# Kernel tuning notes

Measured on AMD Instinct MI355X. Metric: run time of the kernel, lower is better.

Reference implementation:

```python
import jax, jax.numpy as jnp
import numpy as np

D_MODEL = 256
N_HEADS = 8


def setup_inputs() -> dict:
    key = jax.random.key(0)
    ks = jax.random.split(key, 12)
    B, S, d, H = 4, 1024, D_MODEL, N_HEADS
    s = 0.02
    return {
        "Q": jax.random.normal(ks[0], (B, S, d), jnp.float32),
        "K": jax.random.normal(ks[1], (B, S, d), jnp.float32),
        "V": jax.random.normal(ks[2], (B, S, d), jnp.float32),
        "Wq": jax.random.normal(ks[3], (d, d * H), jnp.float32) * s,
        "bq": jnp.zeros((d * H,), jnp.float32),
        "Wk": jax.random.normal(ks[4], (d, d * H), jnp.float32) * s,
        "bk": jnp.zeros((d * H,), jnp.float32),
        "Wv": jax.random.normal(ks[5], (d, d * H), jnp.float32) * s,
        "bv": jnp.zeros((d * H,), jnp.float32),
        "Wo": jax.random.normal(ks[6], (H * d, d), jnp.float32) * s,
        "bo": jnp.zeros((d,), jnp.float32),
    }


def reference(Q, K, V, Wq, bq, Wk, bk, Wv, bv, Wo, bo):
    B, S, d = Q.shape
    H = N_HEADS
    # projections: [B,S,d] -> [B,S,H*d] -> [B,H,S,d] (head_dim == d_model here)
    q = (Q @ Wq + bq).reshape(B, S, H, d).transpose(0, 2, 1, 3)
    k = (K @ Wk + bk).reshape(B, S, H, d).transpose(0, 2, 1, 3)
    v = (V @ Wv + bv).reshape(B, S, H, d).transpose(0, 2, 1, 3)
    scores = jnp.einsum("bhqd,bhkd->bhqk", q, k) / jnp.sqrt(jnp.float32(d))
    attn = jax.nn.softmax(scores, axis=-1)
    out = jnp.einsum("bhqk,bhkd->bhqd", attn, v)  # [B,H,S,d]
    out = out.transpose(0, 2, 1, 3).reshape(B, S, H * d)
    return out @ Wo + bo
```

## Files before the change

### kernel.cpp

```cpp
#include <hip/hip_runtime.h>
#include <stdint.h>

#define NB 4
#define SEQ 1024
#define DM 256
#define NH 8

typedef __attribute__((ext_vector_type(8))) short bf8;
typedef __attribute__((ext_vector_type(4))) float f4;

__device__ __forceinline__ unsigned short f2bf(float f) {
  union { float f; uint32_t u; } c; c.f = f;
  uint32_t u = c.u;
  return (unsigned short)((u + 0x7FFFu + ((u >> 16) & 1u)) >> 16);
}

__device__ __forceinline__ void gl_lds16(const unsigned short* g, short* l) {
  __builtin_amdgcn_global_load_lds(
      (const __attribute__((address_space(1))) unsigned int*)g,
      (__attribute__((address_space(3))) unsigned int*)l, 16, 0, 0);
}


__global__ __launch_bounds__(256) void prep_kernel(
    const float* __restrict__ Wq, const float* __restrict__ Wk,
    const float* __restrict__ Wv, const float* __restrict__ Wo,
    const float* __restrict__ Q, const float* __restrict__ K,
    const float* __restrict__ V,
    unsigned short* __restrict__ Wt3, unsigned short* __restrict__ WoT,
    unsigned short* __restrict__ Xbf) {
  const int tid = threadIdx.x;
  const int bid = blockIdx.x;

#pragma unroll
  for (int it = 0; it < 6; ++it) {
    const int idx = (it * 512 + bid) * 256 + tid;
    const int z = idx >> 18;
    const int r = idx & 262143;
    const float* src = (z == 0) ? Q : (z == 1) ? K : V;
    const float4 v = *(const float4*)(src + (size_t)r * 4);
    short4 s;
    s.x = (short)f2bf(v.x); s.y = (short)f2bf(v.y);
    s.z = (short)f2bf(v.z); s.w = (short)f2bf(v.w);
    *(short4*)(Xbf + (size_t)z * 1048576 + (size_t)r * 4) = s;
  }

  __shared__ float t[32][33];
  const int tx = tid & 31, ty = tid >> 5;
  for (int tt = 0; tt < 4; ++tt) {
    const int id = bid * 4 + tt;
    const float* in;
    unsigned short* out;
    int R, C, bx, by;
    if (id < 1536) {
      const int z = id >> 9, rem = id & 511;
      in = (z == 0) ? Wq : (z == 1) ? Wk : Wv;
      out = Wt3 + (size_t)z * 2048 * 256;
      R = 256; C = 2048; bx = rem & 63; by = rem >> 6;
    } else {
      const int rem = id - 1536;
      in = Wo; out = WoT;
      R = 2048; C = 256; bx = rem & 7; by = rem >> 3;
    }
    const int c0 = bx * 32, r0 = by * 32;
    __syncthreads();
#pragma unroll
    for (int i = 0; i < 4; i++) {
      int r = r0 + ty + i * 8;
      t[ty + i * 8][tx] = in[(size_t)r * C + c0 + tx];
    }
    __syncthreads();
#pragma unroll
    for (int i = 0; i < 4; i++) {
      int c = c0 + ty + i * 8;
      out[(size_t)c * R + r0 + tx] = f2bf(t[tx][ty + i * 8]);
    }
  }
}

__global__ __launch_bounds__(256) void proj_kernel(
    const unsigned short* __restrict__ Xbf, const unsigned short* __restrict__ Wt3,
    const float* __restrict__ bq, const float* __restrict__ bk, const float* __restrict__ bv,
    unsigned short* __restrict__ q_frag, unsigned short* __restrict__ k_frag,
    unsigned short* __restrict__ v_frag) {
  const int z = blockIdx.z;
  const unsigned short* X = Xbf + (size_t)z * 4096 * 256;
  const unsigned short* Wt = Wt3 + (size_t)z * 2048 * 256;
  const float* bias = (z == 0) ? bq : (z == 1) ? bk : bv;

  __shared__ short a_lds[128 * 64];
  __shared__ short b_lds[128 * 64];

  const int tid = threadIdx.x;
  const int wid = tid >> 6, lane = tid & 63;
  const int quad = lane >> 4, l16 = lane & 15;
  const int wm = wid >> 1, wn = wid & 1;
  const int m0 = blockIdx.x * 128, n0 = blockIdx.y * 128;

  f4 acc[4][4];
  const f4 z4 = {0.f, 0.f, 0.f, 0.f};
#pragma unroll
  for (int i = 0; i < 4; i++)
#pragma unroll
    for (int j = 0; j < 4; j++) acc[i][j] = z4;

  const int srow = lane >> 2;
  const int schunk = lane & 3;
  const int cxor = quad ^ (l16 & 3);

  for (int ko = 0; ko < 4; ko++) {
    const int k0 = ko * 64;
#pragma unroll
    for (int jj = 0; jj < 4; jj++) {
      const int c = wid * 4 + jj;
      const int kh = c >> 3, i = c & 7;
      const int row = i * 16 + srow;
      const int sc = (schunk ^ (row & 3)) * 8;
      gl_lds16(X + (size_t)(m0 + row) * DM + k0 + kh * 32 + sc, a_lds + c * 512);
      gl_lds16(Wt + (size_t)(n0 + row) * DM + k0 + kh * 32 + sc, b_lds + c * 512);
    }
    __syncthreads();
#pragma unroll
    for (int kh = 0; kh < 2; kh++) {
      bf8 af[4], bfv[4];
#pragma unroll
      for (int mi = 0; mi < 4; mi++)
        af[mi] = *(const bf8*)(a_lds + kh * 4096 + (wm * 64 + mi * 16 + l16) * 32 + cxor * 8);
#pragma unroll
      for (int ni = 0; ni < 4; ni++)
        bfv[ni] = *(const bf8*)(b_lds + kh * 4096 + (wn * 64 + ni * 16 + l16) * 32 + cxor * 8);
      if (z < 2) {
#pragma unroll
        for (int ni = 0; ni < 4; ni++)
#pragma unroll
          for (int mi = 0; mi < 4; mi++)
            acc[ni][mi] = __builtin_amdgcn_mfma_f32_16x16x32_bf16(bfv[ni], af[mi], acc[ni][mi], 0, 0, 0);
      } else {
#pragma unroll
        for (int mi = 0; mi < 4; mi++)
#pragma unroll
          for (int ni = 0; ni < 4; ni++)
            acc[mi][ni] = __builtin_amdgcn_mfma_f32_16x16x32_bf16(af[mi], bfv[ni], acc[mi][ni], 0, 0, 0);
      }
    }
    __syncthreads();
  }

  if (z < 2) {
    const float scale = (z == 0) ? 0.0901684400f : 1.0f;
    unsigned short* dst = (z == 0) ? q_frag : k_frag;
#pragma unroll
    for (int ni = 0; ni < 4; ni++) {
      const int nb = n0 + wn * 64 + ni * 16 + quad * 4;
      const float4 b4 = *(const float4*)(bias + nb);
      const int h = nb >> 8, dd = nb & 255;
      const int dq = (dd >> 3) & 3, jh = dd & 7;
#pragma unroll
      for (int mi = 0; mi < 4; mi++) {
        const int tok = m0 + wm * 64 + mi * 16 + l16;
        const int b = tok >> 10, sr = tok & 1023;
        const size_t idx = ((size_t)(b * NH + h) * 64 + (sr >> 4)) * 4096 +
                           (size_t)(dd >> 5) * 512 + ((sr & 15) + 16 * dq) * 8 + jh;
        short4 s4;
        s4.x = (short)f2bf((acc[ni][mi][0] + b4.x) * scale);
        s4.y = (short)f2bf((acc[ni][mi][1] + b4.y) * scale);
        s4.z = (short)f2bf((acc[ni][mi][2] + b4.z) * scale);
        s4.w = (short)f2bf((acc[ni][mi][3] + b4.w) * scale);
        *(short4*)(dst + idx) = s4;
      }
    }
  } else {
#pragma unroll
    for (int ni = 0; ni < 4; ni++) {
      const int n = n0 + wn * 64 + ni * 16 + l16;
      const float bsv = bias[n];
      const int h = n >> 8, d = n & 255;
#pragma unroll
      for (int mi = 0; mi < 4; mi++) {
        const int m = m0 + wm * 64 + mi * 16 + quad * 4;
        const int b = m >> 10, sr = m & 1023;
        const size_t idx = ((size_t)(b * NH + h) * 16 + (d >> 4)) * 16384 +
                           (size_t)(sr >> 5) * 512 +
                           ((d & 15) + 16 * ((sr >> 3) & 3)) * 8 + (sr & 7);
        short4 s4;
        s4.x = (short)f2bf(acc[mi][ni][0] + bsv);
        s4.y = (short)f2bf(acc[mi][ni][1] + bsv);
        s4.z = (short)f2bf(acc[mi][ni][2] + bsv);
        s4.w = (short)f2bf(acc[mi][ni][3] + bsv);
        *(short4*)(v_frag + idx) = s4;
      }
    }
  }
}

__global__ __launch_bounds__(256) void attn_kernel(
    const unsigned short* __restrict__ q_frag, const unsigned short* __restrict__ k_frag,
    const unsigned short* __restrict__ v_frag, unsigned short* __restrict__ o_ws) {
  __shared__ short k_lds[2][8192];
  __shared__ short p_lds[2][64][40];
  __shared__ float l_sh[64];

  const int tid = threadIdx.x;
  const int wid = tid >> 6, lane = tid & 63;
  const int quad = lane >> 4, l16 = lane & 15;
  const int blk = blockIdx.x;
  const int g = blk & 7;
  const int qt = (blk >> 3) & 15;
  const int bh = g + 8 * (blk >> 7);
  const size_t fbase = (size_t)bh * 262144;

  bf8 qf[8];
  {
    const unsigned short* qp = q_frag + fbase + (size_t)(qt * 4 + wid) * 4096 + lane * 8;
#pragma unroll
    for (int kc = 0; kc < 8; kc++) qf[kc] = *(const bf8*)(qp + kc * 512);
  }

  const f4 z4 = {0.f, 0.f, 0.f, 0.f};
  f4 Oacc[4][4];
#pragma unroll
  for (int i = 0; i < 4; i++)
#pragma unroll
    for (int j = 0; j < 4; j++) Oacc[i][j] = z4;
  float lpart[4] = {0.f, 0.f, 0.f, 0.f};

  const unsigned short* kdma_src = k_frag + fbase + (size_t)wid * 2048 + lane * 8;
#pragma unroll
  for (int jj = 0; jj < 4; jj++)
    gl_lds16(kdma_src + jj * 512, &k_lds[0][wid * 2048 + jj * 512]);
  __syncthreads();

  bf8 vpre0[4], vpre1[4];
  const unsigned short* vbase_p = v_frag + fbase + (size_t)(wid * 4) * 16384 + lane * 8;

#define ATTN_STEP(T, CUR, PRV, VCUR, VPRV)                                     \
  {                                                                            \
    const int t_ = (T);                                                        \
    _Pragma("unroll")                                                          \
    for (int mi = 0; mi < 4; mi++)                                             \
      VCUR[mi] = *(const bf8*)(vbase_p + (size_t)mi * 16384 + (size_t)t_ * 512); \
    f4 Sacc[2];                                                                \
    Sacc[0] = z4; Sacc[1] = z4;                                                \
    _Pragma("unroll")                                                          \
    for (int kc = 0; kc < 8; kc++) {                                           \
      const bf8 aq = qf[kc];                                                   \
      _Pragma("unroll")                                                        \
      for (int ni = 0; ni < 2; ni++) {                                         \
        const bf8 kb = *(const bf8*)(&k_lds[CUR][(ni * 8 + kc) * 512 + lane * 8]); \
        Sacc[ni] = __builtin_amdgcn_mfma_f32_16x16x32_bf16(aq, kb, Sacc[ni], 0, 0, 0); \
      }                                                                        \
    }                                                                          \
    if (t_ < 31) {                                                             \
      _Pragma("unroll")                                                        \
      for (int jj = 0; jj < 4; jj++)                                           \
        gl_lds16(kdma_src + (size_t)(t_ + 1) * 8192 + jj * 512,                \
                 &k_lds[PRV][wid * 2048 + jj * 512]);                          \
    }                                                                          \
    if (t_ > 0) {                                                              \
      bf8 pb[4];                                                               \
      _Pragma("unroll")                                                        \
      for (int nq = 0; nq < 4; nq++)                                           \
        pb[nq] = *(const bf8*)(&p_lds[PRV][nq * 16 + l16][quad * 8]);          \
      _Pragma("unroll")                                                        \
      for (int mi = 0; mi < 4; mi++)                                           \
        _Pragma("unroll")                                                      \
        for (int nq = 0; nq < 4; nq++)                                         \
          Oacc[mi][nq] = __builtin_amdgcn_mfma_f32_16x16x32_bf16(VPRV[mi], pb[nq], Oacc[mi][nq], 0, 0, 0); \
    }                                                                          \
    _Pragma("unroll")                                                          \
    for (int reg = 0; reg < 4; reg++) {                                        \
      const int qrow = wid * 16 + quad * 4 + reg;                              \
      float s = 0.f;                                                           \
      _Pragma("unroll")                                                        \
      for (int ni = 0; ni < 2; ni++) {                                         \
        const float p = exp2f(Sacc[ni][reg]);                                  \
        s += p;                                                                \
        union { float f; uint32_t u; } c;                                      \
        c.f = p;                                                               \
        p_lds[CUR][qrow][ni * 16 + l16] = (short)((c.u + 0x8000u) >> 16);      \
      }                                                                        \
      lpart[reg] += s;                                                         \
    }                                                                          \
    __syncthreads();                                                           \
  }

  for (int tt = 0; tt < 16; tt++) {
    ATTN_STEP(tt * 2, 0, 1, vpre0, vpre1)
    ATTN_STEP(tt * 2 + 1, 1, 0, vpre1, vpre0)
  }
#undef ATTN_STEP

  {
    bf8 pb[4];
#pragma unroll
    for (int nq = 0; nq < 4; nq++)
      pb[nq] = *(const bf8*)(&p_lds[1][nq * 16 + l16][quad * 8]);
#pragma unroll
    for (int mi = 0; mi < 4; mi++)
#pragma unroll
      for (int nq = 0; nq < 4; nq++)
        Oacc[mi][nq] = __builtin_amdgcn_mfma_f32_16x16x32_bf16(vpre1[mi], pb[nq], Oacc[mi][nq], 0, 0, 0);
  }

#pragma unroll
  for (int reg = 0; reg < 4; reg++) {
    float v = lpart[reg];
    v += __shfl_xor(v, 1, 64);
    v += __shfl_xor(v, 2, 64);
    v += __shfl_xor(v, 4, 64);
    v += __shfl_xor(v, 8, 64);
    if (l16 == 0) l_sh[wid * 16 + quad * 4 + reg] = v;
  }
  __syncthreads();

  const int b = bh >> 3, h = bh & 7;
#pragma unroll
  for (int nq = 0; nq < 4; nq++) {
    const int q = nq * 16 + l16;
    const float inv = 1.f / l_sh[q];
    const size_t base = ((size_t)b * SEQ + qt * 64 + q) * (NH * DM) + h * DM + wid * 64;
#pragma unroll
    for (int mi = 0; mi < 4; mi++) {
      short4 s4;
      s4.x = (short)f2bf(Oacc[mi][nq][0] * inv);
      s4.y = (short)f2bf(Oacc[mi][nq][1] * inv);
      s4.z = (short)f2bf(Oacc[mi][nq][2] * inv);
      s4.w = (short)f2bf(Oacc[mi][nq][3] * inv);
      *(short4*)(o_ws + base + mi * 16 + quad * 4) = s4;
    }
  }
}

__global__ __launch_bounds__(256) void outproj_kernel(
    const unsigned short* __restrict__ o_ws, const unsigned short* __restrict__ WoT,
    const float* __restrict__ bo, float* __restrict__ out) {
  __shared__ short a_lds[32][264];
  __shared__ short b_lds[64][264];

  const int tid = threadIdx.x;
  const int wid = tid >> 6, lane = tid & 63;
  const int quad = lane >> 4, l16 = lane & 15;
  const int wm = wid & 1, wn = wid >> 1;
  const int m0 = blockIdx.x * 32, n0 = blockIdx.y * 64;

  const f4 z4 = {0.f, 0.f, 0.f, 0.f};
  f4 acc[2];
#pragma unroll
  for (int i = 0; i < 2; i++) acc[i] = z4;

  const int ch = tid & 31, row = tid >> 5;
  for (int ko = 0; ko < 8; ko++) {
    const int k0 = ko * 256;
#pragma unroll
    for (int rb = 0; rb < 4; rb++) {
      int r = row + rb * 8;
      *(bf8*)(&a_lds[r][ch * 8]) = *(const bf8*)(o_ws + (size_t)(m0 + r) * 2048 + k0 + ch * 8);
    }
#pragma unroll
    for (int rb = 0; rb < 8; rb++) {
      int r = row + rb * 8;
      *(bf8*)(&b_lds[r][ch * 8]) = *(const bf8*)(WoT + (size_t)(n0 + r) * 2048 + k0 + ch * 8);
    }
    __syncthreads();
#pragma unroll
    for (int kc = 0; kc < 8; kc++) {
      const bf8 af = *(const bf8*)(&a_lds[wm * 16 + l16][kc * 32 + quad * 8]);
      bf8 bfv[2];
#pragma unroll
      for (int ni = 0; ni < 2; ni++)
        bfv[ni] = *(const bf8*)(&b_lds[wn * 32 + ni * 16 + l16][kc * 32 + quad * 8]);
#pragma unroll
      for (int ni = 0; ni < 2; ni++)
        acc[ni] = __builtin_amdgcn_mfma_f32_16x16x32_bf16(af, bfv[ni], acc[ni], 0, 0, 0);
    }
    __syncthreads();
  }
#pragma unroll
  for (int ni = 0; ni < 2; ni++) {
    const int n = n0 + wn * 32 + ni * 16 + l16;
    const float bv = bo[n];
#pragma unroll
    for (int reg = 0; reg < 4; reg++) {
      const int m = m0 + wm * 16 + quad * 4 + reg;
      out[(size_t)m * DM + n] = acc[ni][reg] + bv;
    }
  }
}

extern "C" void kernel_launch(void* const* d_in, const int* in_sizes, int n_in,
                              void* d_out, int out_size, void* d_ws, size_t ws_size,
                              hipStream_t stream) {
  const float* Q  = (const float*)d_in[0];
  const float* K  = (const float*)d_in[1];
  const float* V  = (const float*)d_in[2];
  const float* Wq = (const float*)d_in[3];
  const float* bq = (const float*)d_in[4];
  const float* Wk = (const float*)d_in[5];
  const float* bk = (const float*)d_in[6];
  const float* Wv = (const float*)d_in[7];
  const float* bv = (const float*)d_in[8];
  const float* Wo = (const float*)d_in[9];
  const float* bo = (const float*)d_in[10];
  float* out = (float*)d_out;

  char* ws = (char*)d_ws;
  const size_t QS = (size_t)NB * NH * SEQ * DM * 2;
  unsigned short* q_frag = (unsigned short*)(ws);
  unsigned short* k_frag = (unsigned short*)(ws + QS);
  unsigned short* v_frag = (unsigned short*)(ws + 2 * QS);
  unsigned short* o_ws   = (unsigned short*)(ws + 3 * QS);
  const size_t WT = (size_t)2048 * 256 * 2;
  unsigned short* Wt3 = (unsigned short*)(ws + 4 * QS);
  unsigned short* WoT = (unsigned short*)(ws + 4 * QS + 3 * WT);
  unsigned short* Xbf = o_ws;

  prep_kernel<<<512, 256, 0, stream>>>(Wq, Wk, Wv, Wo, Q, K, V,
                                       Wt3, WoT, Xbf);
  proj_kernel<<<dim3(32, 16, 3), 256, 0, stream>>>(Xbf, Wt3, bq, bk, bv,
                                                   q_frag, k_frag, v_frag);
  attn_kernel<<<512, 256, 0, stream>>>(q_frag, k_frag, v_frag, o_ws);
  outproj_kernel<<<dim3(128, 4), 256, 0, stream>>>(o_ws, WoT, bo, out);
}
```

Before: 166.9 us.

## Fuse four kernels into one persistent kernel with grid barriers

```diff
diff --git a/kernel.cpp b/kernel.cpp
--- a/kernel.cpp
+++ b/kernel.cpp
@@ -21,217 +21,230 @@
       (__attribute__((address_space(3))) unsigned int*)l, 16, 0, 0);
 }
 
-
-__global__ __launch_bounds__(256) void prep_kernel(
-    const float* __restrict__ Wq, const float* __restrict__ Wk,
-    const float* __restrict__ Wv, const float* __restrict__ Wo,
-    const float* __restrict__ Q, const float* __restrict__ K,
-    const float* __restrict__ V,
-    unsigned short* __restrict__ Wt3, unsigned short* __restrict__ WoT,
-    unsigned short* __restrict__ Xbf) {
+__device__ __forceinline__ void grid_barrier(unsigned* cnt, unsigned nblk) {
+  __threadfence();
+  __syncthreads();
+  if (threadIdx.x == 0) {
+    atomicAdd(cnt, 1u);
+    unsigned spins = 0;
+    while (atomicAdd(cnt, 0u) < nblk) {
+      __builtin_amdgcn_s_sleep(8);
+      if (++spins > 10000000u) break;
+    }
+  }
+  __syncthreads();
+  __threadfence();
+}
+
+union SMemU {
+  struct { float t[32][33]; } prep;
+  struct { short a[128 * 64]; short b[128 * 64]; } proj;
+  struct { short k[2][8192]; short p[2][64][40]; float l[64]; } attn;
+  struct { short a[32][136]; short b[64][136]; } oproj;
+};
+
+__global__ __launch_bounds__(256, 2) void fused_kernel(
+    const float* Wq, const float* Wk, const float* Wv, const float* Wo,
+    const float* Q, const float* K, const float* V,
+    const float* bq, const float* bk, const float* bv, const float* bo,
+    unsigned short* Wt3, unsigned short* WoT, unsigned short* Xbf,
+    unsigned short* q_frag, unsigned short* k_frag, unsigned short* v_frag,
+    unsigned short* o_ws, float* out, unsigned* bar) {
+  __shared__ alignas(16) SMemU sm;
+
   const int tid = threadIdx.x;
   const int bid = blockIdx.x;
-
-#pragma unroll
-  for (int it = 0; it < 6; ++it) {
-    const int idx = (it * 512 + bid) * 256 + tid;
-    const int z = idx >> 18;
-    const int r = idx & 262143;
-    const float* src = (z == 0) ? Q : (z == 1) ? K : V;
-    const float4 v = *(const float4*)(src + (size_t)r * 4);
-    short4 s;
-    s.x = (short)f2bf(v.x); s.y = (short)f2bf(v.y);
-    s.z = (short)f2bf(v.z); s.w = (short)f2bf(v.w);
-    *(short4*)(Xbf + (size_t)z * 1048576 + (size_t)r * 4) = s;
-  }
-
-  __shared__ float t[32][33];
-  const int tx = tid & 31, ty = tid >> 5;
-  for (int tt = 0; tt < 4; ++tt) {
-    const int id = bid * 4 + tt;
-    const float* in;
-    unsigned short* out;
-    int R, C, bx, by;
-    if (id < 1536) {
-      const int z = id >> 9, rem = id & 511;
-      in = (z == 0) ? Wq : (z == 1) ? Wk : Wv;
-      out = Wt3 + (size_t)z * 2048 * 256;
-      R = 256; C = 2048; bx = rem & 63; by = rem >> 6;
-    } else {
-      const int rem = id - 1536;
-      in = Wo; out = WoT;
-      R = 2048; C = 256; bx = rem & 7; by = rem >> 3;
-    }
-    const int c0 = bx * 32, r0 = by * 32;
-    __syncthreads();
-#pragma unroll
-    for (int i = 0; i < 4; i++) {
-      int r = r0 + ty + i * 8;
-      t[ty + i * 8][tx] = in[(size_t)r * C + c0 + tx];
-    }
-    __syncthreads();
-#pragma unroll
-    for (int i = 0; i < 4; i++) {
-      int c = c0 + ty + i * 8;
-      out[(size_t)c * R + r0 + tx] = f2bf(t[tx][ty + i * 8]);
-    }
-  }
-}
-
-__global__ __launch_bounds__(256) void proj_kernel(
-    const unsigned short* __restrict__ Xbf, const unsigned short* __restrict__ Wt3,
-    const float* __restrict__ bq, const float* __restrict__ bk, const float* __restrict__ bv,
-    unsigned short* __restrict__ q_frag, unsigned short* __restrict__ k_frag,
-    unsigned short* __restrict__ v_frag) {
-  const int z = blockIdx.z;
-  const unsigned short* X = Xbf + (size_t)z * 4096 * 256;
-  const unsigned short* Wt = Wt3 + (size_t)z * 2048 * 256;
-  const float* bias = (z == 0) ? bq : (z == 1) ? bk : bv;
-
-  __shared__ short a_lds[128 * 64];
-  __shared__ short b_lds[128 * 64];
-
-  const int tid = threadIdx.x;
   const int wid = tid >> 6, lane = tid & 63;
   const int quad = lane >> 4, l16 = lane & 15;
-  const int wm = wid >> 1, wn = wid & 1;
-  const int m0 = blockIdx.x * 128, n0 = blockIdx.y * 128;
-
-  f4 acc[4][4];
   const f4 z4 = {0.f, 0.f, 0.f, 0.f};
-#pragma unroll
-  for (int i = 0; i < 4; i++)
-#pragma unroll
-    for (int j = 0; j < 4; j++) acc[i][j] = z4;
-
-  const int srow = lane >> 2;
-  const int schunk = lane & 3;
-  const int cxor = quad ^ (l16 & 3);
-
-  for (int ko = 0; ko < 4; ko++) {
-    const int k0 = ko * 64;
-#pragma unroll
-    for (int jj = 0; jj < 4; jj++) {
-      const int c = wid * 4 + jj;
-      const int kh = c >> 3, i = c & 7;
-      const int row = i * 16 + srow;
-      const int sc = (schunk ^ (row & 3)) * 8;
-      gl_lds16(X + (size_t)(m0 + row) * DM + k0 + kh * 32 + sc, a_lds + c * 512);
-      gl_lds16(Wt + (size_t)(n0 + row) * DM + k0 + kh * 32 + sc, b_lds + c * 512);
-    }
+
+  {
+#pragma unroll
+    for (int it = 0; it < 6; ++it) {
+      const int idx = (it * 512 + bid) * 256 + tid;
+      const int z = idx >> 18;
+      const int r = idx & 262143;
+      const float* src = (z == 0) ? Q : (z == 1) ? K : V;
+      const float4 v = *(const float4*)(src + (size_t)r * 4);
+      short4 s;
+      s.x = (short)f2bf(v.x); s.y = (short)f2bf(v.y);
+      s.z = (short)f2bf(v.z); s.w = (short)f2bf(v.w);
+      *(short4*)(Xbf + (size_t)z * 1048576 + (size_t)r * 4) = s;
+    }
+    float (*t)[33] = sm.prep.t;
+    const int tx = tid & 31, ty = tid >> 5;
+    for (int tt = 0; tt < 4; ++tt) {
+      const int id = bid * 4 + tt;
+      const float* in;
+      unsigned short* outp;
+      int R, C, bx, by;
+      if (id < 1536) {
+        const int z = id >> 9, rem = id & 511;
+        in = (z == 0) ? Wq : (z == 1) ? Wk : Wv;
+        outp = Wt3 + (size_t)z * 2048 * 256;
+        R = 256; C = 2048; bx = rem & 63; by = rem >> 6;
+      } else {
+        const int rem = id - 1536;
+        in = Wo; outp = WoT;
+        R = 2048; C = 256; bx = rem & 7; by = rem >> 3;
+      }
+      const int c0 = bx * 32, r0 = by * 32;
+      __syncthreads();
+#pragma unroll
+      for (int i = 0; i < 4; i++) {
+        int r = r0 + ty + i * 8;
+        t[ty + i * 8][tx] = in[(size_t)r * C + c0 + tx];
+      }
+      __syncthreads();
+#pragma unroll
+      for (int i = 0; i < 4; i++) {
+        int c = c0 + ty + i * 8;
+        outp[(size_t)c * R + r0 + tx] = f2bf(t[tx][ty + i * 8]);
+      }
+    }
+  }
+  grid_barrier(bar + 0, 512);
+
+  {
+    short* a_lds = sm.proj.a;
+    short* b_lds = sm.proj.b;
+    const int bx = bid & 31, by = bid >> 5;
+    const int m0 = bx * 128, n0 = by * 128;
+    const int wm = wid >> 1, wn = wid & 1;
+    const int srow = lane >> 2, schunk = lane & 3;
+    const int cxor = quad ^ (l16 & 3);
+
+    for (int z = 0; z < 3; z++) {
+      const unsigned short* X = Xbf + (size_t)z * 1048576;
+      const unsigned short* Wt = Wt3 + (size_t)z * 524288;
+      const float* bias = (z == 0) ? bq : (z == 1) ? bk : bv;
+
+      f4 acc[4][4];
+#pragma unroll
+      for (int i = 0; i < 4; i++)
+#pragma unroll
+        for (int j = 0; j < 4; j++) acc[i][j] = z4;
+
+      for (int ko = 0; ko < 4; ko++) {
+        const int k0 = ko * 64;
+#pragma unroll
+        for (int jj = 0; jj < 4; jj++) {
+          const int c = wid * 4 + jj;
+          const int kh = c >> 3, i = c & 7;
+          const int row = i * 16 + srow;
+          const int sc = (schunk ^ (row & 3)) * 8;
+          gl_lds16(X + (size_t)(m0 + row) * DM + k0 + kh * 32 + sc, a_lds + c * 512);
+          gl_lds16(Wt + (size_t)(n0 + row) * DM + k0 + kh * 32 + sc, b_lds + c * 512);
+        }
+        __syncthreads();
+#pragma unroll
+        for (int kh = 0; kh < 2; kh++) {
+          bf8 af[4], bfv[4];
+#pragma unroll
+          for (int mi = 0; mi < 4; mi++)
+            af[mi] = *(const bf8*)(a_lds + kh * 4096 + (wm * 64 + mi * 16 + l16) * 32 + cxor * 8);
+#pragma unroll
+          for (int ni = 0; ni < 4; ni++)
+            bfv[ni] = *(const bf8*)(b_lds + kh * 4096 + (wn * 64 + ni * 16 + l16) * 32 + cxor * 8);
+          if (z < 2) {
+#pragma unroll
+            for (int ni = 0; ni < 4; ni++)
+#pragma unroll
+              for (int mi = 0; mi < 4; mi++)
+                acc[ni][mi] = __builtin_amdgcn_mfma_f32_16x16x32_bf16(bfv[ni], af[mi], acc[ni][mi], 0, 0, 0);
+          } else {
+#pragma unroll
+            for (int mi = 0; mi < 4; mi++)
+#pragma unroll
+              for (int ni = 0; ni < 4; ni++)
+                acc[mi][ni] = __builtin_amdgcn_mfma_f32_16x16x32_bf16(af[mi], bfv[ni], acc[mi][ni], 0, 0, 0);
+          }
+        }
+        __syncthreads();
+      }
+
+      if (z < 2) {
+        const float scale = (z == 0) ? 0.0901684400f : 1.0f;
+        unsigned short* dst = (z == 0) ? q_frag : k_frag;
+#pragma unroll
+        for (int ni = 0; ni < 4; ni++) {
+          const int nb = n0 + wn * 64 + ni * 16 + quad * 4;
+          const float4 b4 = *(const float4*)(bias + nb);
+          const int h = nb >> 8, dd = nb & 255;
+          const int dq = (dd >> 3) & 3, jh = dd & 7;
+#pragma unroll
+          for (int mi = 0; mi < 4; mi++) {
+            const int tok = m0 + wm * 64 + mi * 16 + l16;
+            const int b = tok >> 10, sr = tok & 1023;
+            const size_t idx = ((size_t)(b * NH + h) * 64 + (sr >> 4)) * 4096 +
+                               (size_t)(dd >> 5) * 512 + ((sr & 15) + 16 * dq) * 8 + jh;
+            short4 s4;
+            s4.x = (short)f2bf((acc[ni][mi][0] + b4.x) * scale);
+            s4.y = (short)f2bf((acc[ni][mi][1] + b4.y) * scale);
+            s4.z = (short)f2bf((acc[ni][mi][2] + b4.z) * scale);
+            s4.w = (short)f2bf((acc[ni][mi][3] + b4.w) * scale);
+            *(short4*)(dst + idx) = s4;
+          }
+        }
+      } else {
+#pragma unroll
+        for (int ni = 0; ni < 4; ni++) {
+          const int n = n0 + wn * 64 + ni * 16 + l16;
+          const float bsv = bias[n];
+          const int h = n >> 8, d = n & 255;
+#pragma unroll
+          for (int mi = 0; mi < 4; mi++) {
+            const int m = m0 + wm * 64 + mi * 16 + quad * 4;
+            const int b = m >> 10, sr = m & 1023;
+            const size_t idx = ((size_t)(b * NH + h) * 16 + (d >> 4)) * 16384 +
+                               (size_t)(sr >> 5) * 512 +
+                               ((d & 15) + 16 * ((sr >> 3) & 3)) * 8 + (sr & 7);
+            short4 s4;
+            s4.x = (short)f2bf(acc[mi][ni][0] + bsv);
+            s4.y = (short)f2bf(acc[mi][ni][1] + bsv);
+            s4.z = (short)f2bf(acc[mi][ni][2] + bsv);
+            s4.w = (short)f2bf(acc[mi][ni][3] + bsv);
+            *(short4*)(v_frag + idx) = s4;
+          }
+        }
+      }
+    }
+  }
+  grid_barrier(bar + 1, 512);
+
+  {
+    short (*k_lds)[8192] = sm.attn.k;
+    short (*p_lds)[64][40] = sm.attn.p;
+    float* l_sh = sm.attn.l;
+
+    const int blk = bid;
+    const int g = blk & 7;
+    const int qt = (blk >> 3) & 15;
+    const int bh = g + 8 * (blk >> 7);
+    const size_t fbase = (size_t)bh * 262144;
+
+    bf8 qf[8];
+    {
+      const unsigned short* qp = q_frag + fbase + (size_t)(qt * 4 + wid) * 4096 + lane * 8;
+#pragma unroll
+      for (int kc = 0; kc < 8; kc++) qf[kc] = *(const bf8*)(qp + kc * 512);
+    }
+
+    f4 Oacc[4][4];
+#pragma unroll
+    for (int i = 0; i < 4; i++)
+#pragma unroll
+      for (int j = 0; j < 4; j++) Oacc[i][j] = z4;
+    float lpart[4] = {0.f, 0.f, 0.f, 0.f};
+
+    const unsigned short* kdma_src = k_frag + fbase + (size_t)wid * 2048 + lane * 8;
+#pragma unroll
+    for (int jj = 0; jj < 4; jj++)
+      gl_lds16(kdma_src + jj * 512, &k_lds[0][wid * 2048 + jj * 512]);
     __syncthreads();
-#pragma unroll
-    for (int kh = 0; kh < 2; kh++) {
-      bf8 af[4], bfv[4];
-#pragma unroll
-      for (int mi = 0; mi < 4; mi++)
-        af[mi] = *(const bf8*)(a_lds + kh * 4096 + (wm * 64 + mi * 16 + l16) * 32 + cxor * 8);
-#pragma unroll
-      for (int ni = 0; ni < 4; ni++)
-        bfv[ni] = *(const bf8*)(b_lds + kh * 4096 + (wn * 64 + ni * 16 + l16) * 32 + cxor * 8);
-      if (z < 2) {
-#pragma unroll
-        for (int ni = 0; ni < 4; ni++)
-#pragma unroll
-          for (int mi = 0; mi < 4; mi++)
-            acc[ni][mi] = __builtin_amdgcn_mfma_f32_16x16x32_bf16(bfv[ni], af[mi], acc[ni][mi], 0, 0, 0);
-      } else {
-#pragma unroll
-        for (int mi = 0; mi < 4; mi++)
-#pragma unroll
-          for (int ni = 0; ni < 4; ni++)
-            acc[mi][ni] = __builtin_amdgcn_mfma_f32_16x16x32_bf16(af[mi], bfv[ni], acc[mi][ni], 0, 0, 0);
-      }
-    }
-    __syncthreads();
-  }
-
-  if (z < 2) {
-    const float scale = (z == 0) ? 0.0901684400f : 1.0f;
-    unsigned short* dst = (z == 0) ? q_frag : k_frag;
-#pragma unroll
-    for (int ni = 0; ni < 4; ni++) {
-      const int nb = n0 + wn * 64 + ni * 16 + quad * 4;
-      const float4 b4 = *(const float4*)(bias + nb);
-      const int h = nb >> 8, dd = nb & 255;
-      const int dq = (dd >> 3) & 3, jh = dd & 7;
-#pragma unroll
-      for (int mi = 0; mi < 4; mi++) {
-        const int tok = m0 + wm * 64 + mi * 16 + l16;
-        const int b = tok >> 10, sr = tok & 1023;
-        const size_t idx = ((size_t)(b * NH + h) * 64 + (sr >> 4)) * 4096 +
-                           (size_t)(dd >> 5) * 512 + ((sr & 15) + 16 * dq) * 8 + jh;
-        short4 s4;
-        s4.x = (short)f2bf((acc[ni][mi][0] + b4.x) * scale);
-        s4.y = (short)f2bf((acc[ni][mi][1] + b4.y) * scale);
-        s4.z = (short)f2bf((acc[ni][mi][2] + b4.z) * scale);
-        s4.w = (short)f2bf((acc[ni][mi][3] + b4.w) * scale);
-        *(short4*)(dst + idx) = s4;
-      }
-    }
-  } else {
-#pragma unroll
-    for (int ni = 0; ni < 4; ni++) {
-      const int n = n0 + wn * 64 + ni * 16 + l16;
-      const float bsv = bias[n];
-      const int h = n >> 8, d = n & 255;
-#pragma unroll
-      for (int mi = 0; mi < 4; mi++) {
-        const int m = m0 + wm * 64 + mi * 16 + quad * 4;
-        const int b = m >> 10, sr = m & 1023;
-        const size_t idx = ((size_t)(b * NH + h) * 16 + (d >> 4)) * 16384 +
-                           (size_t)(sr >> 5) * 512 +
-                           ((d & 15) + 16 * ((sr >> 3) & 3)) * 8 + (sr & 7);
-        short4 s4;
-        s4.x = (short)f2bf(acc[mi][ni][0] + bsv);
-        s4.y = (short)f2bf(acc[mi][ni][1] + bsv);
-        s4.z = (short)f2bf(acc[mi][ni][2] + bsv);
-        s4.w = (short)f2bf(acc[mi][ni][3] + bsv);
-        *(short4*)(v_frag + idx) = s4;
-      }
-    }
-  }
-}
-
-__global__ __launch_bounds__(256) void attn_kernel(
-    const unsigned short* __restrict__ q_frag, const unsigned short* __restrict__ k_frag,
-    const unsigned short* __restrict__ v_frag, unsigned short* __restrict__ o_ws) {
-  __shared__ short k_lds[2][8192];
-  __shared__ short p_lds[2][64][40];
-  __shared__ float l_sh[64];
-
-  const int tid = threadIdx.x;
-  const int wid = tid >> 6, lane = tid & 63;
-  const int quad = lane >> 4, l16 = lane & 15;
-  const int blk = blockIdx.x;
-  const int g = blk & 7;
-  const int qt = (blk >> 3) & 15;
-  const int bh = g + 8 * (blk >> 7);
-  const size_t fbase = (size_t)bh * 262144;
-
-  bf8 qf[8];
-  {
-    const unsigned short* qp = q_frag + fbase + (size_t)(qt * 4 + wid) * 4096 + lane * 8;
-#pragma unroll
-    for (int kc = 0; kc < 8; kc++) qf[kc] = *(const bf8*)(qp + kc * 512);
-  }
-
-  const f4 z4 = {0.f, 0.f, 0.f, 0.f};
-  f4 Oacc[4][4];
-#pragma unroll
-  for (int i = 0; i < 4; i++)
-#pragma unroll
-    for (int j = 0; j < 4; j++) Oacc[i][j] = z4;
-  float lpart[4] = {0.f, 0.f, 0.f, 0.f};
-
-  const unsigned short* kdma_src = k_frag + fbase + (size_t)wid * 2048 + lane * 8;
-#pragma unroll
-  for (int jj = 0; jj < 4; jj++)
-    gl_lds16(kdma_src + jj * 512, &k_lds[0][wid * 2048 + jj * 512]);
-  __syncthreads();
-
-  bf8 vpre0[4], vpre1[4];
-  const unsigned short* vbase_p = v_frag + fbase + (size_t)(wid * 4) * 16384 + lane * 8;
+
+    bf8 vpre0[4], vpre1[4];
+    const unsigned short* vbase_p = v_frag + fbase + (size_t)(wid * 4) * 16384 + lane * 8;
 
 #define ATTN_STEP(T, CUR, PRV, VCUR, VPRV)                                     \
   {                                                                            \
@@ -284,105 +297,101 @@
     __syncthreads();                                                           \
   }
 
-  for (int tt = 0; tt < 16; tt++) {
-    ATTN_STEP(tt * 2, 0, 1, vpre0, vpre1)
-    ATTN_STEP(tt * 2 + 1, 1, 0, vpre1, vpre0)
-  }
+    for (int tt = 0; tt < 16; tt++) {
+      ATTN_STEP(tt * 2, 0, 1, vpre0, vpre1)
+      ATTN_STEP(tt * 2 + 1, 1, 0, vpre1, vpre0)
+    }
 #undef ATTN_STEP
 
+    {
+      bf8 pb[4];
+#pragma unroll
+      for (int nq = 0; nq < 4; nq++)
+        pb[nq] = *(const bf8*)(&p_lds[1][nq * 16 + l16][quad * 8]);
+#pragma unroll
+      for (int mi = 0; mi < 4; mi++)
+#pragma unroll
+        for (int nq = 0; nq < 4; nq++)
+          Oacc[mi][nq] = __builtin_amdgcn_mfma_f32_16x16x32_bf16(vpre1[mi], pb[nq], Oacc[mi][nq], 0, 0, 0);
+    }
+
+#pragma unroll
+    for (int reg = 0; reg < 4; reg++) {
+      float v = lpart[reg];
+      v += __shfl_xor(v, 1, 64);
+      v += __shfl_xor(v, 2, 64);
+      v += __shfl_xor(v, 4, 64);
+      v += __shfl_xor(v, 8, 64);
+      if (l16 == 0) l_sh[wid * 16 + quad * 4 + reg] = v;
+    }
+    __syncthreads();
+
+    const int b = bh >> 3, h = bh & 7;
+#pragma unroll
+    for (int nq = 0; nq < 4; nq++) {
+      const int q = nq * 16 + l16;
+      const float inv = 1.f / l_sh[q];
+      const size_t base = ((size_t)b * SEQ + qt * 64 + q) * (NH * DM) + h * DM + wid * 64;
+#pragma unroll
+      for (int mi = 0; mi < 4; mi++) {
+        short4 s4;
+        s4.x = (short)f2bf(Oacc[mi][nq][0] * inv);
+        s4.y = (short)f2bf(Oacc[mi][nq][1] * inv);
+        s4.z = (short)f2bf(Oacc[mi][nq][2] * inv);
+        s4.w = (short)f2bf(Oacc[mi][nq][3] * inv);
+        *(short4*)(o_ws + base + mi * 16 + quad * 4) = s4;
+      }
+    }
+  }
+  grid_barrier(bar + 2, 512);
+
   {
-    bf8 pb[4];
-#pragma unroll
-    for (int nq = 0; nq < 4; nq++)
-      pb[nq] = *(const bf8*)(&p_lds[1][nq * 16 + l16][quad * 8]);
-#pragma unroll
-    for (int mi = 0; mi < 4; mi++)
-#pragma unroll
-      for (int nq = 0; nq < 4; nq++)
-        Oacc[mi][nq] = __builtin_amdgcn_mfma_f32_16x16x32_bf16(vpre1[mi], pb[nq], Oacc[mi][nq], 0, 0, 0);
-  }
-
-#pragma unroll
-  for (int reg = 0; reg < 4; reg++) {
-    float v = lpart[reg];
-    v += __shfl_xor(v, 1, 64);
-    v += __shfl_xor(v, 2, 64);
-    v += __shfl_xor(v, 4, 64);
-    v += __shfl_xor(v, 8, 64);
-    if (l16 == 0) l_sh[wid * 16 + quad * 4 + reg] = v;
-  }
-  __syncthreads();
-
-  const int b = bh >> 3, h = bh & 7;
-#pragma unroll
-  for (int nq = 0; nq < 4; nq++) {
-    const int q = nq * 16 + l16;
-    const float inv = 1.f / l_sh[q];
-    const size_t base = ((size_t)b * SEQ + qt * 64 + q) * (NH * DM) + h * DM + wid * 64;
-#pragma unroll
-    for (int mi = 0; mi < 4; mi++) {
-      short4 s4;
-      s4.x = (short)f2bf(Oacc[mi][nq][0] * inv);
-      s4.y = (short)f2bf(Oacc[mi][nq][1] * inv);
-      s4.z = (short)f2bf(Oacc[mi][nq][2] * inv);
-      s4.w = (short)f2bf(Oacc[mi][nq][3] * inv);
-      *(short4*)(o_ws + base + mi * 16 + quad * 4) = s4;
-    }
-  }
-}
-
-__global__ __launch_bounds__(256) void outproj_kernel(
-    const unsigned short* __restrict__ o_ws, const unsigned short* __restrict__ WoT,
-    const float* __restrict__ bo, float* __restrict__ out) {
-  __shared__ short a_lds[32][264];
-  __shared__ short b_lds[64][264];
-
-  const int tid = threadIdx.x;
-  const int wid = tid >> 6, lane = tid & 63;
-  const int quad = lane >> 4, l16 = lane & 15;
-  const int wm = wid & 1, wn = wid >> 1;
-  const int m0 = blockIdx.x * 32, n0 = blockIdx.y * 64;
-
-  const f4 z4 = {0.f, 0.f, 0.f, 0.f};
-  f4 acc[2];
-#pragma unroll
-  for (int i = 0; i < 2; i++) acc[i] = z4;
-
-  const int ch = tid & 31, row = tid >> 5;
-  for (int ko = 0; ko < 8; ko++) {
-    const int k0 = ko * 256;
-#pragma unroll
-    for (int rb = 0; rb < 4; rb++) {
-      int r = row + rb * 8;
-      *(bf8*)(&a_lds[r][ch * 8]) = *(const bf8*)(o_ws + (size_t)(m0 + r) * 2048 + k0 + ch * 8);
-    }
-#pragma unroll
-    for (int rb = 0; rb < 8; rb++) {
-      int r = row + rb * 8;
-      *(bf8*)(&b_lds[r][ch * 8]) = *(const bf8*)(WoT + (size_t)(n0 + r) * 2048 + k0 + ch * 8);
-    }
-    __syncthreads();
-#pragma unroll
-    for (int kc = 0; kc < 8; kc++) {
-      const bf8 af = *(const bf8*)(&a_lds[wm * 16 + l16][kc * 32 + quad * 8]);
-      bf8 bfv[2];
-#pragma unroll
-      for (int ni = 0; ni < 2; ni++)
-        bfv[ni] = *(const bf8*)(&b_lds[wn * 32 + ni * 16 + l16][kc * 32 + quad * 8]);
-#pragma unroll
-      for (int ni = 0; ni < 2; ni++)
-        acc[ni] = __builtin_amdgcn_mfma_f32_16x16x32_bf16(af, bfv[ni], acc[ni], 0, 0, 0);
-    }
-    __syncthreads();
-  }
-#pragma unroll
-  for (int ni = 0; ni < 2; ni++) {
-    const int n = n0 + wn * 32 + ni * 16 + l16;
-    const float bv = bo[n];
-#pragma unroll
-    for (int reg = 0; reg < 4; reg++) {
-      const int m = m0 + wm * 16 + quad * 4 + reg;
-      out[(size_t)m * DM + n] = acc[ni][reg] + bv;
+    short (*a_lds)[136] = sm.oproj.a;
+    short (*b_lds)[136] = sm.oproj.b;
+    const int bx = bid & 127, by = bid >> 7;
+    const int wm = wid & 1, wn = wid >> 1;
+    const int m0 = bx * 32, n0 = by * 64;
+
+    f4 acc[2];
+#pragma unroll
+    for (int i = 0; i < 2; i++) acc[i] = z4;
+
+    const int ch = tid & 15, row = tid >> 4;
+    for (int ko = 0; ko < 16; ko++) {
+      const int k0 = ko * 128;
+#pragma unroll
+      for (int rb = 0; rb < 2; rb++) {
+        int r = row + rb * 16;
+        *(bf8*)(&a_lds[r][ch * 8]) = *(const bf8*)(o_ws + (size_t)(m0 + r) * 2048 + k0 + ch * 8);
+      }
+#pragma unroll
+      for (int rb = 0; rb < 4; rb++) {
+        int r = row + rb * 16;
+        *(bf8*)(&b_lds[r][ch * 8]) = *(const bf8*)(WoT + (size_t)(n0 + r) * 2048 + k0 + ch * 8);
+      }
+      __syncthreads();
+#pragma unroll
+      for (int kc = 0; kc < 4; kc++) {
+        const bf8 af = *(const bf8*)(&a_lds[wm * 16 + l16][kc * 32 + quad * 8]);
+        bf8 bfv[2];
+#pragma unroll
+        for (int ni = 0; ni < 2; ni++)
+          bfv[ni] = *(const bf8*)(&b_lds[wn * 32 + ni * 16 + l16][kc * 32 + quad * 8]);
+#pragma unroll
+        for (int ni = 0; ni < 2; ni++)
+          acc[ni] = __builtin_amdgcn_mfma_f32_16x16x32_bf16(af, bfv[ni], acc[ni], 0, 0, 0);
+      }
+      __syncthreads();
+    }
+#pragma unroll
+    for (int ni = 0; ni < 2; ni++) {
+      const int n = n0 + wn * 32 + ni * 16 + l16;
+      const float bv = bo[n];
+#pragma unroll
+      for (int reg = 0; reg < 4; reg++) {
+        const int m = m0 + wm * 16 + quad * 4 + reg;
+        out[(size_t)m * DM + n] = acc[ni][reg] + bv;
+      }
     }
   }
 }
@@ -405,19 +414,20 @@
 
   char* ws = (char*)d_ws;
   const size_t QS = (size_t)NB * NH * SEQ * DM * 2;
+  const size_t WT = (size_t)2048 * 256 * 2;
   unsigned short* q_frag = (unsigned short*)(ws);
   unsigned short* k_frag = (unsigned short*)(ws + QS);
   unsigned short* v_frag = (unsigned short*)(ws + 2 * QS);
   unsigned short* o_ws   = (unsigned short*)(ws + 3 * QS);
-  const size_t WT = (size_t)2048 * 256 * 2;
   unsigned short* Wt3 = (unsigned short*)(ws + 4 * QS);
   unsigned short* WoT = (unsigned short*)(ws + 4 * QS + 3 * WT);
-  unsigned short* Xbf = o_ws;
-
-  prep_kernel<<<512, 256, 0, stream>>>(Wq, Wk, Wv, Wo, Q, K, V,
-                                       Wt3, WoT, Xbf);
-  proj_kernel<<<dim3(32, 16, 3), 256, 0, stream>>>(Xbf, Wt3, bq, bk, bv,
-                                                   q_frag, k_frag, v_frag);
-  attn_kernel<<<512, 256, 0, stream>>>(q_frag, k_frag, v_frag, o_ws);
-  outproj_kernel<<<dim3(128, 4), 256, 0, stream>>>(o_ws, WoT, bo, out);
+  unsigned short* Xbf = (unsigned short*)(ws + 4 * QS + 4 * WT);
+  unsigned* bar = (unsigned*)(ws + 4 * QS + 4 * WT + 3 * 2097152);
+
+  hipMemsetAsync(bar, 0, 256, stream);
+  fused_kernel<<<512, 256, 0, stream>>>(Wq, Wk, Wv, Wo, Q, K, V,
+                                        bq, bk, bv, bo,
+                                        Wt3, WoT, Xbf,
+                                        q_frag, k_frag, v_frag,
+                                        o_ws, out, bar);
 }
```

Measured after the change: 496.8 us. 198% more time.
